# Kernel optimization log

Hardware: AMD Instinct MI355X
Metric: run time of the kernel (lower is better)

Reference implementation:

```python
import jax, jax.numpy as jnp
import numpy as np

VOCAB = 50000
EMB = 128
HID = 256
OUT = 1


def setup_inputs() -> dict:
    key = jax.random.key(0)
    ks = jax.random.split(key, 8)
    B, T = 256, 512
    s_emb = 1.0 / np.sqrt(EMB)
    s_hid = 1.0 / np.sqrt(HID)
    return {
        "x": jax.random.randint(ks[0], (B, T), 0, VOCAB, dtype=jnp.int32),
        "emb_table": jax.random.normal(ks[1], (VOCAB, EMB), dtype=jnp.float32),
        "W_ih": jax.random.uniform(ks[2], (4 * HID, EMB), jnp.float32, -s_hid, s_hid),
        "W_hh": jax.random.uniform(ks[3], (4 * HID, HID), jnp.float32, -s_hid, s_hid),
        "b_ih": jax.random.uniform(ks[4], (4 * HID,), jnp.float32, -s_hid, s_hid),
        "b_hh": jax.random.uniform(ks[5], (4 * HID,), jnp.float32, -s_hid, s_hid),
        "W_fc": jax.random.uniform(ks[6], (OUT, HID), jnp.float32, -s_hid, s_hid),
        "b_fc": jax.random.uniform(ks[7], (OUT,), jnp.float32, -s_hid, s_hid),
    }


def _lstm_last_hidden(embedded, W_ih, W_hh, b_ih, b_hh):
    # embedded: [B, T, E]; PyTorch gate order: i, f, g, o
    B = embedded.shape[0]
    H = W_hh.shape[1]
    # precompute input projections for all timesteps: [T, B, 4H]
    x_proj = jnp.einsum('bte,ge->tbg', embedded, W_ih) + b_ih + b_hh

    def step(carry, xp):
        h, c = carry
        gates = xp + h @ W_hh.T  # [B, 4H]
        i, f, g, o = jnp.split(gates, 4, axis=-1)
        i = jax.nn.sigmoid(i)
        f = jax.nn.sigmoid(f)
        g = jnp.tanh(g)
        o = jax.nn.sigmoid(o)
        c = f * c + i * g
        h = o * jnp.tanh(c)
        return (h, c), None

    h0 = jnp.zeros((B, H), embedded.dtype)
    c0 = jnp.zeros((B, H), embedded.dtype)
    (h_last, _), _ = jax.lax.scan(step, (h0, c0), x_proj)
    return h_last  # [B, H] == lstm_out[:, -1, :]


def reference(x, emb_table, W_ih, W_hh, b_ih, b_hh, W_fc, b_fc):
    embedded = emb_table[x]  # [B, T, E]
    h_last = _lstm_last_hidden(embedded, W_ih, W_hh, b_ih, b_hh)
    logits = h_last @ W_fc.T + b_fc  # [B, OUT]
    return jax.nn.sigmoid(logits)
```

## Files before the change

kernel.cpp:

```cpp
#include <hip/hip_runtime.h>
#include <hip/hip_bf16.h>
#include <stdint.h>

#define VOCAB 50000
#define EMB   128
#define HID   256
#define G4    1024
#define BATCH 256
#define SEQ   512
#define LOG2E 1.4426950408889634f

typedef __attribute__((ext_vector_type(8))) short bf16x8;
typedef __attribute__((ext_vector_type(4))) float f32x4;
typedef __attribute__((ext_vector_type(4))) int   i32x4;
typedef __attribute__((ext_vector_type(2))) unsigned u32x2;

__device__ __forceinline__ ushort f2bf(float f) {
  uint32_t u; __builtin_memcpy(&u, &f, 4);
  uint32_t r = (u + 0x7fffu + ((u >> 16) & 1u)) >> 16;
  return (ushort)r;
}
__device__ __forceinline__ float asf(uint32_t x) {
  float f; __builtin_memcpy(&f, &x, 4);
  return f;
}
__device__ __forceinline__ float rcp(float x) { return __builtin_amdgcn_rcpf(x); }
__device__ __forceinline__ float ex2(float x) { return __builtin_amdgcn_exp2f(x); }

#define WAIT_LGKM() asm volatile("s_waitcnt lgkmcnt(0)" ::: "memory")
#define RAW_BAR()  do { __builtin_amdgcn_sched_barrier(0); \
                        __builtin_amdgcn_s_barrier(); \
                        __builtin_amdgcn_sched_barrier(0); } while (0)

__global__ __launch_bounds__(256) void k_proj(
    const float* __restrict__ emb, const float* __restrict__ W_ih,
    const float* __restrict__ b_ih, const float* __restrict__ b_hh,
    ushort* __restrict__ proj) {
  const int lane = threadIdx.x & 63;
  const int wv = threadIdx.x >> 6;
  const int vbase = (blockIdx.x * 4 + wv) * 64;
  const int lm = lane & 15, lq = lane >> 4;
  const int nt0 = blockIdx.y * 32;

  bf16x8 A[4][4];
  #pragma unroll
  for (int mt = 0; mt < 4; ++mt) {
    int v = vbase + mt * 16 + lm;
    int vc = v < VOCAB ? v : 0;
    const float* rp = emb + (size_t)vc * EMB;
    #pragma unroll
    for (int kt = 0; kt < 4; ++kt) {
      const float* p = rp + kt * 32 + lq * 8;
      #pragma unroll
      for (int i = 0; i < 8; ++i) A[mt][kt][i] = (short)f2bf(p[i]);
    }
  }
  for (int ntl = 0; ntl < 32; ++ntl) {
    const int g = (nt0 + ntl) * 16 + lm;
    const int newcol = (g & 255) * 4 + (g >> 8);
    bf16x8 B[4];
    #pragma unroll
    for (int kt = 0; kt < 4; ++kt) {
      const float* p = W_ih + (size_t)g * EMB + kt * 32 + lq * 8;
      #pragma unroll
      for (int i = 0; i < 8; ++i) B[kt][i] = (short)f2bf(p[i]);
    }
    const float bias = b_ih[g] + b_hh[g];
    #pragma unroll
    for (int mt = 0; mt < 4; ++mt) {
      f32x4 acc = {0.f, 0.f, 0.f, 0.f};
      #pragma unroll
      for (int kt = 0; kt < 4; ++kt)
        acc = __builtin_amdgcn_mfma_f32_16x16x32_bf16(A[mt][kt], B[kt], acc, 0, 0, 0);
      #pragma unroll
      for (int r = 0; r < 4; ++r) {
        int row = vbase + mt * 16 + lq * 4 + r;
        if (row < VOCAB) proj[(size_t)row * G4 + newcol] = f2bf((acc[r] + bias) * LOG2E);
      }
    }
  }
}

__global__ __launch_bounds__(256) void k_w2(const float* __restrict__ Whh,
                                            int* __restrict__ W2) {
  const int f = blockIdx.x * 256 + threadIdx.x;
  const int lane = f & 63, kc = (f >> 6) & 3, nt = (f >> 8) & 7, wv = (f >> 11) & 7;
  const int grow = (nt >> 1) * 256 + wv * 32 + (nt & 1) * 16 + (lane & 15);
  const int k0 = kc * 64 + (lane >> 4) * 16;
  const float* src = Whh + (size_t)grow * HID + k0;
  unsigned d[4];
  #pragma unroll
  for (int dw = 0; dw < 4; ++dw) {
    unsigned acc = 0;
    #pragma unroll
    for (int b = 0; b < 4; ++b) {
      int q = (int)rintf(src[dw * 4 + b] * 2032.f);
      q = q > 127 ? 127 : (q < -127 ? -127 : q);
      acc |= ((unsigned)q & 0xffu) << (8 * b);
    }
    d[dw] = acc;
  }
  i32x4 o = {(int)d[0], (int)d[1], (int)d[2], (int)d[3]};
  *(i32x4*)(W2 + (size_t)f * 4) = o;
}

__global__ __launch_bounds__(512, 2) void k_lstm(
    const int* __restrict__ x, const ushort* __restrict__ proj,
    const int* __restrict__ W2, const float* __restrict__ W_fc,
    const float* __restrict__ b_fc, float* __restrict__ out) {
  __shared__ __align__(16) char hbuf[2][544];
  __shared__ __align__(16) int xlds[SEQ * 2];
  __shared__ float red[8][2];

  const int tid = threadIdx.x;
  const int lane = tid & 63, wv = tid >> 6;
  const int lm = lane & 15, lq = lane >> 4;
  const int b0 = blockIdx.x * 2;
  const int js = (lane >> 4) & 1;
  const int b = lane >> 5;
  const int jme = wv * 32 + js * 16 + lm;
  const int bsel = (lm >> 2) & 1;
  const int bpaddr = (((lane >> 5) << 4) | lm) * 4;

  i32x4 Wf[8][4];
  {
    const i32x4* wb = (const i32x4*)W2;
    #pragma unroll
    for (int nt = 0; nt < 8; ++nt)
      #pragma unroll
      for (int kc = 0; kc < 4; ++kc)
        Wf[nt][kc] = wb[wv * 2048 + nt * 256 + kc * 64 + lane];
    #pragma unroll
    for (int nt = 0; nt < 8; ++nt)
      #pragma unroll
      for (int kc = 0; kc < 4; ++kc)
        asm volatile("" : "+a"(Wf[nt][kc]));
  }

  for (int i = tid; i < SEQ * 2; i += 512) {
    int bl = i >> 9, t = i & 511;
    xlds[t * 2 + bl] = x[(b0 + bl) * SEQ + t];
  }
  for (int i = tid; i < 272; i += 512) ((int*)hbuf)[i] = 0;

  float c = 0.f, hl = 0.f;

  __syncthreads();

  u32x2 xp0, xp1;
  {
    int i0 = xlds[b];
    xp0 = *(const u32x2*)(proj + (size_t)i0 * G4 + jme * 4);
    int i1 = xlds[2 + b];
    xp1 = *(const u32x2*)(proj + (size_t)i1 * G4 + jme * 4);
  }

  const float S2 = LOG2E / 258064.f;

#define GATE_PHASE(G, DOMFMA, XP, GV)                                         \
  {                                                                           \
    i32x4 a0 = {0, 0, 0, 0}, a1 = {0, 0, 0, 0};                               \
    if (DOMFMA) {                                                             \
      _Pragma("unroll")                                                       \
      for (int kc = 0; kc < 4; ++kc) {                                        \
        a0 = __builtin_amdgcn_mfma_i32_16x16x64_i8(A[kc], Wf[2*(G)][kc], a0, 0, 0, 0);   \
        a1 = __builtin_amdgcn_mfma_i32_16x16x64_i8(A[kc], Wf[2*(G)+1][kc], a1, 0, 0, 0); \
      }                                                                       \
    }                                                                         \
    int v0 = __builtin_amdgcn_ds_bpermute(bpaddr, a0[0]);                     \
    int v1 = __builtin_amdgcn_ds_bpermute(bpaddr, a1[0]);                     \
    int av = js ? v1 : v0;                                                    \
    unsigned w_ = ((G) < 2) ? XP[0] : XP[1];                                  \
    unsigned bits_ = ((G) & 1) ? (w_ & 0xffff0000u) : (w_ << 16);             \
    GV = (float)av * S2 + asf(bits_);                                         \
  }

#define STEP(T, RB, WB, DOMFMA, XP)                                           \
  {                                                                           \
    i32x4 A[4];                                                               \
    if (DOMFMA) {                                                             \
      const char* hb_ = hbuf[RB];                                             \
      _Pragma("unroll")                                                       \
      for (int kc = 0; kc < 4; ++kc)                                          \
        A[kc] = *(const i32x4*)(hb_ + bsel * 272 + kc * 64 + lq * 16);        \
    }                                                                         \
    float gv_;                                                                \
    GATE_PHASE(2, DOMFMA, XP, gv_);                               \
    float eg_ = ex2(gv_ + gv_);                                               \
    float tg_ = (eg_ - 1.f) * rcp(eg_ + 1.f);                                 \
    GATE_PHASE(0, DOMFMA, XP, gv_);                               \
    float si_ = rcp(1.f + ex2(-gv_));                                         \
    float sitg_ = si_ * tg_;                                                  \
    GATE_PHASE(1, DOMFMA, XP, gv_);                               \
    float sf_ = rcp(1.f + ex2(-gv_));                                         \
    float cn_ = sf_ * c + sitg_;                                              \
    c = cn_;                                                                  \
    float e2_ = ex2(cn_ * (2.f * LOG2E));                                     \
    float tc_ = 1.f - 2.f * rcp(e2_ + 1.f);                      \
    GATE_PHASE(3, DOMFMA, XP, gv_);                               \
    float so_ = rcp(1.f + ex2(-gv_));                                         \
    float h_ = so_ * tc_;                                                     \
    hl = h_;                                                                  \
    int q_ = (int)rintf(h_ * 127.f);                                          \
    hbuf[WB][b * 272 + jme] = (char)q_;                                       \
    {                                                     \
      int t2_ = ((T) + 2 < SEQ) ? (T) + 2 : SEQ - 1;                          \
      int idx_ = xlds[t2_ * 2 + b];                                           \
      XP = *(const u32x2*)(proj + (size_t)idx_ * G4 + jme * 4);               \
    }                                                                         \
    WAIT_LGKM();                                                              \
    RAW_BAR();                                                                \
  }

  STEP(0, 0, 1, false, xp0);
  #pragma clang loop unroll(disable)
  for (int tt = 0; tt < 255; ++tt) {
    STEP(2 * tt + 1, 1, 0, true, xp1);
    STEP(2 * tt + 2, 0, 1, true, xp0);
  }
  STEP(511, 1, 0, true, xp1);

  float p = hl * W_fc[jme];
  p += __shfl_xor(p, 1);
  p += __shfl_xor(p, 2);
  p += __shfl_xor(p, 4);
  p += __shfl_xor(p, 8);
  p += __shfl_xor(p, 16);
  if ((lane & 31) == 0) red[wv][b] = p;
  __syncthreads();
  if (tid < 2) {
    float s = 0.f;
    #pragma unroll
    for (int w = 0; w < 8; ++w) s += red[w][tid];
    s += b_fc[0];
    out[b0 + tid] = rcp(1.f + ex2(-s * LOG2E));
  }
}

extern "C" void kernel_launch(void* const* d_in, const int* in_sizes, int n_in,
                              void* d_out, int out_size, void* d_ws, size_t ws_size,
                              hipStream_t stream) {
  const int*   x    = (const int*)d_in[0];
  const float* emb  = (const float*)d_in[1];
  const float* W_ih = (const float*)d_in[2];
  const float* W_hh = (const float*)d_in[3];
  const float* b_ih = (const float*)d_in[4];
  const float* b_hh = (const float*)d_in[5];
  const float* W_fc = (const float*)d_in[6];
  const float* b_fc = (const float*)d_in[7];
  float* out = (float*)d_out;

  char* ws = (char*)d_ws;
  ushort* proj = (ushort*)ws;
  int*    W2   = (int*)(ws + 102400000);

  k_proj<<<dim3(196, 2), dim3(256), 0, stream>>>(emb, W_ih, b_ih, b_hh, proj);
  k_w2<<<dim3(64), dim3(256), 0, stream>>>(W_hh, W2);
  k_lstm<<<dim3(128), dim3(512), 0, stream>>>(x, proj, W2, W_fc, b_fc, out);
}
```

Before: 522.6 us.

## Replace int8 MFMA recurrence with per-thread sdot4 GEMV, one batch per block

```diff
diff --git a/kernel.cpp b/kernel.cpp
--- a/kernel.cpp
+++ b/kernel.cpp
@@ -13,7 +13,6 @@
 typedef __attribute__((ext_vector_type(8))) short bf16x8;
 typedef __attribute__((ext_vector_type(4))) float f32x4;
 typedef __attribute__((ext_vector_type(4))) int   i32x4;
-typedef __attribute__((ext_vector_type(2))) unsigned u32x2;
 
 __device__ __forceinline__ ushort f2bf(float f) {
   uint32_t u; __builtin_memcpy(&u, &f, 4);
@@ -82,158 +81,147 @@
 }
 
 __global__ __launch_bounds__(256) void k_w2(const float* __restrict__ Whh,
-                                            int* __restrict__ W2) {
-  const int f = blockIdx.x * 256 + threadIdx.x;
-  const int lane = f & 63, kc = (f >> 6) & 3, nt = (f >> 8) & 7, wv = (f >> 11) & 7;
-  const int grow = (nt >> 1) * 256 + wv * 32 + (nt & 1) * 16 + (lane & 15);
-  const int k0 = kc * 64 + (lane >> 4) * 16;
-  const float* src = Whh + (size_t)grow * HID + k0;
+                                            int* __restrict__ W3) {
+  const int t = blockIdx.x * 256 + threadIdx.x;
+  const int lane = t & 63, c = t >> 6;
+  const int kq = c & 15, wv = (c >> 4) & 7, v = c >> 7;
+  const int gp = lane >> 5;
+  const int j = wv * 32 + (lane & 31);
+  const int g = gp * 2 + v;
+  const float* src = Whh + (size_t)(g * 256 + j) * HID + kq * 16;
   unsigned d[4];
   #pragma unroll
-  for (int dw = 0; dw < 4; ++dw) {
+  for (int e = 0; e < 4; ++e) {
     unsigned acc = 0;
     #pragma unroll
     for (int b = 0; b < 4; ++b) {
-      int q = (int)rintf(src[dw * 4 + b] * 2032.f);
+      int q = (int)rintf(src[e * 4 + b] * 2032.f);
       q = q > 127 ? 127 : (q < -127 ? -127 : q);
       acc |= ((unsigned)q & 0xffu) << (8 * b);
     }
-    d[dw] = acc;
+    d[e] = acc;
   }
   i32x4 o = {(int)d[0], (int)d[1], (int)d[2], (int)d[3]};
-  *(i32x4*)(W2 + (size_t)f * 4) = o;
+  *(i32x4*)(W3 + (size_t)(c * 64 + lane) * 4) = o;
 }
 
 __global__ __launch_bounds__(512, 2) void k_lstm(
     const int* __restrict__ x, const ushort* __restrict__ proj,
-    const int* __restrict__ W2, const float* __restrict__ W_fc,
+    const int* __restrict__ W3, const float* __restrict__ W_fc,
     const float* __restrict__ b_fc, float* __restrict__ out) {
-  __shared__ __align__(16) char hbuf[2][544];
-  __shared__ __align__(16) int xlds[SEQ * 2];
-  __shared__ float red[8][2];
+  __shared__ __align__(16) char hbuf[2][256];
+  __shared__ __align__(16) int xlds[SEQ];
+  __shared__ float red[8];
 
   const int tid = threadIdx.x;
   const int lane = tid & 63, wv = tid >> 6;
-  const int lm = lane & 15, lq = lane >> 4;
-  const int b0 = blockIdx.x * 2;
-  const int js = (lane >> 4) & 1;
-  const int b = lane >> 5;
-  const int jme = wv * 32 + js * 16 + lm;
-  const int bsel = (lm >> 2) & 1;
-  const int bpaddr = (((lane >> 5) << 4) | lm) * 4;
-
-  i32x4 Wf[8][4];
+  const int gp = lane >> 5;
+  const int j = wv * 32 + (lane & 31);
+  const int b0 = blockIdx.x;
+  const int colb = j * 4 + gp * 2;
+
+  i32x4 Wd0[16], Wd1[16];
   {
-    const i32x4* wb = (const i32x4*)W2;
-    #pragma unroll
-    for (int nt = 0; nt < 8; ++nt)
-      #pragma unroll
-      for (int kc = 0; kc < 4; ++kc)
-        Wf[nt][kc] = wb[wv * 2048 + nt * 256 + kc * 64 + lane];
-    #pragma unroll
-    for (int nt = 0; nt < 8; ++nt)
-      #pragma unroll
-      for (int kc = 0; kc < 4; ++kc)
-        asm volatile("" : "+a"(Wf[nt][kc]));
-  }
-
-  for (int i = tid; i < SEQ * 2; i += 512) {
-    int bl = i >> 9, t = i & 511;
-    xlds[t * 2 + bl] = x[(b0 + bl) * SEQ + t];
-  }
-  for (int i = tid; i < 272; i += 512) ((int*)hbuf)[i] = 0;
+    const i32x4* wb = (const i32x4*)W3;
+    #pragma unroll
+    for (int kq = 0; kq < 16; ++kq) {
+      Wd0[kq] = wb[(size_t)((0 * 8 + wv) * 16 + kq) * 64 + lane];
+      Wd1[kq] = wb[(size_t)((1 * 8 + wv) * 16 + kq) * 64 + lane];
+    }
+    #pragma unroll
+    for (int kq = 0; kq < 16; ++kq) {
+      asm volatile("" : "+v"(Wd0[kq]));
+      asm volatile("" : "+v"(Wd1[kq]));
+    }
+  }
+
+  for (int i = tid; i < SEQ; i += 512) xlds[i] = x[b0 * SEQ + i];
+  if (tid < 128) ((int*)hbuf)[tid] = 0;
 
   float c = 0.f, hl = 0.f;
-
   __syncthreads();
 
-  u32x2 xp0, xp1;
-  {
-    int i0 = xlds[b];
-    xp0 = *(const u32x2*)(proj + (size_t)i0 * G4 + jme * 4);
-    int i1 = xlds[2 + b];
-    xp1 = *(const u32x2*)(proj + (size_t)i1 * G4 + jme * 4);
-  }
+  unsigned xp0, xp1;
+  xp0 = *(const unsigned*)(proj + (size_t)xlds[0] * G4 + colb);
+  xp1 = *(const unsigned*)(proj + (size_t)xlds[1] * G4 + colb);
 
   const float S2 = LOG2E / 258064.f;
 
-#define GATE_PHASE(G, DOMFMA, XP, GV)                                         \
+#define STEP(T, RB, WB, XP)                                                   \
   {                                                                           \
-    i32x4 a0 = {0, 0, 0, 0}, a1 = {0, 0, 0, 0};                               \
-    if (DOMFMA) {                                                             \
+    int p0 = 0, p1 = 0, p2 = 0, p3 = 0;                    \
+    int q0 = 0, q1 = 0, q2 = 0, q3 = 0;                    \
+    _Pragma("unroll")                                                         \
+    for (int kh = 0; kh < 2; ++kh) {                                          \
+      i32x4 hq[8];                                                            \
       _Pragma("unroll")                                                       \
-      for (int kc = 0; kc < 4; ++kc) {                                        \
-        a0 = __builtin_amdgcn_mfma_i32_16x16x64_i8(A[kc], Wf[2*(G)][kc], a0, 0, 0, 0);   \
-        a1 = __builtin_amdgcn_mfma_i32_16x16x64_i8(A[kc], Wf[2*(G)+1][kc], a1, 0, 0, 0); \
+      for (int k8 = 0; k8 < 8; ++k8)                                          \
+        hq[k8] = *(const i32x4*)(hbuf[RB] + (kh * 8 + k8) * 16);              \
+      _Pragma("unroll")                                                       \
+      for (int k8 = 0; k8 < 8; ++k8) {                                        \
+        const int kq = kh * 8 + k8;                                           \
+        p0 = __builtin_amdgcn_sdot4(hq[k8][0], Wd0[kq][0], p0, false);        \
+        p1 = __builtin_amdgcn_sdot4(hq[k8][1], Wd0[kq][1], p1, false);        \
+        p2 = __builtin_amdgcn_sdot4(hq[k8][2], Wd0[kq][2], p2, false);        \
+        p3 = __builtin_amdgcn_sdot4(hq[k8][3], Wd0[kq][3], p3, false);        \
+        q0 = __builtin_amdgcn_sdot4(hq[k8][0], Wd1[kq][0], q0, false);        \
+        q1 = __builtin_amdgcn_sdot4(hq[k8][1], Wd1[kq][1], q1, false);        \
+        q2 = __builtin_amdgcn_sdot4(hq[k8][2], Wd1[kq][2], q2, false);        \
+        q3 = __builtin_amdgcn_sdot4(hq[k8][3], Wd1[kq][3], q3, false);        \
       }                                                                       \
     }                                                                         \
-    int v0 = __builtin_amdgcn_ds_bpermute(bpaddr, a0[0]);                     \
-    int v1 = __builtin_amdgcn_ds_bpermute(bpaddr, a1[0]);                     \
-    int av = js ? v1 : v0;                                                    \
-    unsigned w_ = ((G) < 2) ? XP[0] : XP[1];                                  \
-    unsigned bits_ = ((G) & 1) ? (w_ & 0xffff0000u) : (w_ << 16);             \
-    GV = (float)av * S2 + asf(bits_);                                         \
-  }
-
-#define STEP(T, RB, WB, DOMFMA, XP)                                           \
-  {                                                                           \
-    i32x4 A[4];                                                               \
-    if (DOMFMA) {                                                             \
-      const char* hb_ = hbuf[RB];                                             \
-      _Pragma("unroll")                                                       \
-      for (int kc = 0; kc < 4; ++kc)                                          \
-        A[kc] = *(const i32x4*)(hb_ + bsel * 272 + kc * 64 + lq * 16);        \
-    }                                                                         \
-    float gv_;                                                                \
-    GATE_PHASE(2, DOMFMA, XP, gv_);                               \
-    float eg_ = ex2(gv_ + gv_);                                               \
+    int a0 = (p0 + p1) + (p2 + p3);                                           \
+    int a1 = (q0 + q1) + (q2 + q3);                                           \
+    float gv0 = (float)a0 * S2 + asf(XP << 16);                               \
+    float gv1 = (float)a1 * S2 + asf(XP & 0xffff0000u);                       \
+    float og0 = __shfl_xor(gv0, 32);                                          \
+    float og1 = __shfl_xor(gv1, 32);                                          \
+    float gi = gp ? og0 : gv0;                                                \
+    float gf = gp ? og1 : gv1;                                                \
+    float gg = gp ? gv0 : og0;                                                \
+    float go = gp ? gv1 : og1;                                                \
+    float si_ = rcp(1.f + ex2(-gi));                                          \
+    float sf_ = rcp(1.f + ex2(-gf));                                          \
+    float eg_ = ex2(gg + gg);                                                 \
     float tg_ = (eg_ - 1.f) * rcp(eg_ + 1.f);                                 \
-    GATE_PHASE(0, DOMFMA, XP, gv_);                               \
-    float si_ = rcp(1.f + ex2(-gv_));                                         \
-    float sitg_ = si_ * tg_;                                                  \
-    GATE_PHASE(1, DOMFMA, XP, gv_);                               \
-    float sf_ = rcp(1.f + ex2(-gv_));                                         \
-    float cn_ = sf_ * c + sitg_;                                              \
+    float so_ = rcp(1.f + ex2(-go));                                          \
+    float cn_ = sf_ * c + si_ * tg_;                                          \
     c = cn_;                                                                  \
     float e2_ = ex2(cn_ * (2.f * LOG2E));                                     \
-    float tc_ = 1.f - 2.f * rcp(e2_ + 1.f);                      \
-    GATE_PHASE(3, DOMFMA, XP, gv_);                               \
-    float so_ = rcp(1.f + ex2(-gv_));                                         \
+    float tc_ = 1.f - 2.f * rcp(e2_ + 1.f);                                   \
     float h_ = so_ * tc_;                                                     \
     hl = h_;                                                                  \
-    int q_ = (int)rintf(h_ * 127.f);                                          \
-    hbuf[WB][b * 272 + jme] = (char)q_;                                       \
+    if (gp == 0) hbuf[WB][j] = (char)(int)rintf(h_ * 127.f);                  \
     {                                                     \
       int t2_ = ((T) + 2 < SEQ) ? (T) + 2 : SEQ - 1;                          \
-      int idx_ = xlds[t2_ * 2 + b];                                           \
-      XP = *(const u32x2*)(proj + (size_t)idx_ * G4 + jme * 4);               \
+      XP = *(const unsigned*)(proj + (size_t)xlds[t2_] * G4 + colb);          \
     }                                                                         \
     WAIT_LGKM();                                                              \
     RAW_BAR();                                                                \
   }
 
-  STEP(0, 0, 1, false, xp0);
+  STEP(0, 0, 1, xp0);
   #pragma clang loop unroll(disable)
   for (int tt = 0; tt < 255; ++tt) {
-    STEP(2 * tt + 1, 1, 0, true, xp1);
-    STEP(2 * tt + 2, 0, 1, true, xp0);
-  }
-  STEP(511, 1, 0, true, xp1);
-
-  float p = hl * W_fc[jme];
+    STEP(2 * tt + 1, 1, 0, xp1);
+    STEP(2 * tt + 2, 0, 1, xp0);
+  }
+  STEP(511, 1, 0, xp1);
+
+  float p = hl * W_fc[j];
   p += __shfl_xor(p, 1);
   p += __shfl_xor(p, 2);
   p += __shfl_xor(p, 4);
   p += __shfl_xor(p, 8);
   p += __shfl_xor(p, 16);
-  if ((lane & 31) == 0) red[wv][b] = p;
+  if (lane == 0) red[wv] = p;
   __syncthreads();
-  if (tid < 2) {
+  if (tid == 0) {
     float s = 0.f;
     #pragma unroll
-    for (int w = 0; w < 8; ++w) s += red[w][tid];
+    for (int w = 0; w < 8; ++w) s += red[w];
     s += b_fc[0];
-    out[b0 + tid] = rcp(1.f + ex2(-s * LOG2E));
+    out[b0] = rcp(1.f + ex2(-s * LOG2E));
   }
 }
 
@@ -252,9 +240,9 @@
 
   char* ws = (char*)d_ws;
   ushort* proj = (ushort*)ws;
-  int*    W2   = (int*)(ws + 102400000);
+  int*    W3   = (int*)(ws + 102400000);
 
   k_proj<<<dim3(196, 2), dim3(256), 0, stream>>>(emb, W_ih, b_ih, b_hh, proj);
-  k_w2<<<dim3(64), dim3(256), 0, stream>>>(W_hh, W2);
-  k_lstm<<<dim3(128), dim3(512), 0, stream>>>(x, proj, W2, W_fc, b_fc, out);
-}
+  k_w2<<<dim3(64), dim3(256), 0, stream>>>(W_hh, W3);
+  k_lstm<<<dim3(256), dim3(512), 0, stream>>>(x, proj, W3, W_fc, b_fc, out);
+}
```

Measured after the change: 555.6 us. 6.3% more time.
